# Kernel optimization log

Measured on AMD Instinct MI355X. Metric: run time of the kernel, lower is better.

The kernel has to match this reference:

```python
import jax, jax.numpy as jnp
import numpy as np

NBINS = 256
STRENGTH = 100.0  # __init__ strength kwarg


def _hist_channel(x):
    # x: [N] flattened masked channel -> 256-bin histogram over [min,max]
    lo = jnp.min(x)
    hi = jnp.max(x)
    scale = (NBINS - 1) / jnp.maximum(hi - lo, 1e-12)
    bins = jnp.clip(jnp.floor((x - lo) * scale + 0.5).astype(jnp.int32), 0, NBINS - 1)
    return jnp.zeros((NBINS,), dtype=x.dtype).at[bins].add(1.0)


def _match_channel(x, t_hist):
    # CDF-based histogram matching (cpp.matchHistogram): remap sorted values of x
    # to bin centers of the target histogram; output normalized to [0,1].
    N = x.shape[0]
    idx = jnp.argsort(x)
    t = t_hist * (N / jnp.maximum(jnp.sum(t_hist), 1e-12))
    cdf = jnp.cumsum(t)  # [NBINS]
    ranks = jnp.arange(N, dtype=cdf.dtype) + 0.5
    bins = jnp.clip(jnp.searchsorted(cdf, ranks), 0, NBINS - 1)
    vals = bins.astype(x.dtype) / (NBINS - 1)
    return jnp.zeros_like(x).at[idx].set(vals)


def reference(input, masks, target_hists, target_mins, target_maxs):
    # input: [1,C,H,W]; masks: [S,H,W]; target_hists: [S,C,256]; mins/maxs: [S,C]
    C = input.shape[1]
    x = input[0]  # [C,H,W]

    def per_style(mask, t_hist, t_min, t_max):
        mf = (x * mask[None]).reshape(C, -1)  # masked feature, [C,N]
        hist = jax.vmap(_hist_channel)(mf)    # computed every call (as in source)
        matched = jax.vmap(_match_channel)(mf, t_hist)  # [C,N] in [0,1]
        target = matched * (t_max - t_min)[:, None] + t_min[:, None]
        target = jax.lax.stop_gradient(target)  # torch uses .data (detached)
        loss = 0.01 * STRENGTH * jnp.mean((mf - target) ** 2)  # nn.MSELoss
        return loss, hist

    losses, hists = jax.vmap(per_style)(masks, target_hists, target_mins, target_maxs)
    return jnp.sum(losses), hists


def setup_inputs() -> dict:
    key = jax.random.key(0)
    k1, k2, k3, k4 = jax.random.split(key, 4)
    S, C, H, W = 2, 256, 256, 256
    input = jax.random.normal(k1, (1, C, H, W), dtype=jnp.float32)
    masks = (jax.random.uniform(k2, (S, H, W)) > 0.5).astype(jnp.float32)
    target_hists = jax.random.uniform(k3, (S, C, NBINS), dtype=jnp.float32) * 100.0
    base = jax.random.normal(k4, (S, C), dtype=jnp.float32)
    target_mins = base - 1.0
    target_maxs = base + 1.0
    return {"input": input, "masks": masks, "target_hists": target_hists,
            "target_mins": target_mins, "target_maxs": target_maxs}
```

## Files before the change

kernel.cpp:

```cpp
#include <hip/hip_runtime.h>
#include <math.h>

#define NBINS 256
#define NB    4096
#define NCOPY 4
#define BLKT  1024

__global__ void mask_bits_kernel(const float* __restrict__ masks,
                                 unsigned* __restrict__ bits, int total)
{
    const int idx = blockIdx.x * blockDim.x + threadIdx.x;
    bool m = false;
    if (idx < total) m = (masks[idx] != 0.0f);
    const unsigned long long b = __ballot(m);
    const int lane = threadIdx.x & 63;
    if (idx < total) {
        if (lane == 0)       bits[idx >> 5] = (unsigned)b;
        else if (lane == 32) bits[idx >> 5] = (unsigned)(b >> 32);
    }
}

__global__ __launch_bounds__(BLKT, 8) void fused_kernel(
    const float* __restrict__ x, const unsigned* __restrict__ bits,
    const float* __restrict__ thist, const float* __restrict__ tmins,
    const float* __restrict__ tmaxs,
    float* __restrict__ out, float* __restrict__ lossws, int C, int N)
{
    const int nwg = gridDim.x;
    const int orig = blockIdx.x;
    int newid = orig;
    if ((nwg & 7) == 0) newid = (orig & 7) * (nwg >> 3) + (orig >> 3);
    const int c = newid >> 1;
    const int g = newid & 1;

    const float* __restrict__ xc = x + (size_t)c * N;
    const unsigned* __restrict__ wb = bits + (size_t)g * (N >> 5);
    const int tid = threadIdx.x, lane = tid & 63, wid = tid >> 6;

    __shared__ unsigned cntS[NCOPY][NB + 1];
    __shared__ float Sarr[NBINS];
    __shared__ int   Karr[NBINS];
    __shared__ float thsum[4];
    __shared__ unsigned ctot[16];
    __shared__ float wtot[16];
    __shared__ float lsum[4];
    __shared__ float statsS[3];
    __shared__ float wr[3][16];

    const int step16 = BLKT * 16;
    const int Nmain  = (N / step16) * step16;

    float mn = 3.4e38f, mx = -3.4e38f, sq = 0.f;
    for (int i = tid * 16; i < Nmain; i += step16) {
        const float4 a0 = *reinterpret_cast<const float4*>(xc + i);
        const float4 a1 = *reinterpret_cast<const float4*>(xc + i + 4);
        const float4 a2 = *reinterpret_cast<const float4*>(xc + i + 8);
        const float4 a3 = *reinterpret_cast<const float4*>(xc + i + 12);
        const unsigned w = wb[i >> 5] >> (i & 31);
        const float e[16] = { a0.x, a0.y, a0.z, a0.w, a1.x, a1.y, a1.z, a1.w,
                              a2.x, a2.y, a2.z, a2.w, a3.x, a3.y, a3.z, a3.w };
        #pragma unroll
        for (int j = 0; j < 16; ++j) {
            const float v = ((w >> j) & 1u) ? e[j] : 0.0f;
            mn = fminf(mn, v); mx = fmaxf(mx, v); sq += v * v;
        }
    }
    for (int i = Nmain + tid * 4; i < N; i += BLKT * 4) {
        const float4 xv = *reinterpret_cast<const float4*>(xc + i);
        const unsigned w = wb[i >> 5] >> (i & 31);
        const float e[4] = { xv.x, xv.y, xv.z, xv.w };
        #pragma unroll
        for (int j = 0; j < 4; ++j) {
            const float v = ((w >> j) & 1u) ? e[j] : 0.0f;
            mn = fminf(mn, v); mx = fmaxf(mx, v); sq += v * v;
        }
    }
    #pragma unroll
    for (int off = 32; off > 0; off >>= 1) {
        mn = fminf(mn, __shfl_xor(mn, off));
        mx = fmaxf(mx, __shfl_xor(mx, off));
        sq += __shfl_xor(sq, off);
    }
    if (lane == 0) { wr[0][wid] = mn; wr[1][wid] = mx; wr[2][wid] = sq; }

    float th = 0.f, thscan = 0.f;
    if (tid < NBINS) {
        th = thist[(size_t)(g * C + c) * NBINS + tid];
        thscan = th;
        #pragma unroll
        for (int off = 1; off < 64; off <<= 1) {
            const float t = __shfl_up(thscan, off);
            if (lane >= off) thscan += t;
        }
        if (lane == 63) thsum[wid] = thscan;
    }
    {
        unsigned* cf = &cntS[0][0];
        for (int k = tid; k < NCOPY * (NB + 1); k += BLKT) cf[k] = 0u;
    }
    __syncthreads();

    if (tid == 0) {
        float a = wr[0][0], b = wr[1][0], s = wr[2][0];
        for (int k = 1; k < 16; ++k) {
            a = fminf(a, wr[0][k]); b = fmaxf(b, wr[1][k]); s += wr[2][k];
        }
        statsS[0] = a; statsS[1] = b; statsS[2] = s;
    }
    __syncthreads();

    const float lo   = statsS[0];
    const float rng  = fmaxf(statsS[1] - lo, 1e-12f);
    const float sc16 = 4080.0f / rng;
    const float u    = rng / 4080.0f;

    if (tid < NBINS) {
        float cross = 0.f, tsum = 0.f;
        #pragma unroll
        for (int w2 = 0; w2 < 4; ++w2) { if (w2 < wid) cross += thsum[w2]; tsum += thsum[w2]; }
        const float scale = (float)N / fmaxf(tsum, 1e-12f);
        const float cdfv = (thscan + cross) * scale;
        int K = (int)floorf(cdfv - 0.5f) + 1;
        K = min(N, max(0, K));
        if (tid == NBINS - 1) K = N;
        Karr[tid] = K;
    }

    unsigned* __restrict__ cm = cntS[wid >> 2];
    for (int i = tid * 16; i < Nmain; i += step16) {
        const float4 a0 = *reinterpret_cast<const float4*>(xc + i);
        const float4 a1 = *reinterpret_cast<const float4*>(xc + i + 4);
        const float4 a2 = *reinterpret_cast<const float4*>(xc + i + 8);
        const float4 a3 = *reinterpret_cast<const float4*>(xc + i + 12);
        const unsigned w = wb[i >> 5] >> (i & 31);
        const float e[16] = { a0.x, a0.y, a0.z, a0.w, a1.x, a1.y, a1.z, a1.w,
                              a2.x, a2.y, a2.z, a2.w, a3.x, a3.y, a3.z, a3.w };
        #pragma unroll
        for (int j = 0; j < 16; ++j) {
            if ((w >> j) & 1u) {
                const int jb = min(NB - 1, max(0, (int)floorf((e[j] - lo) * sc16 + 8.0f)));
                atomicAdd(&cm[jb], 1u);
            }
        }
    }
    for (int i = Nmain + tid * 4; i < N; i += BLKT * 4) {
        const float4 xv = *reinterpret_cast<const float4*>(xc + i);
        const unsigned w = wb[i >> 5] >> (i & 31);
        const float e[4] = { xv.x, xv.y, xv.z, xv.w };
        #pragma unroll
        for (int j = 0; j < 4; ++j) {
            if ((w >> j) & 1u) {
                const int jb = min(NB - 1, max(0, (int)floorf((e[j] - lo) * sc16 + 8.0f)));
                atomicAdd(&cm[jb], 1u);
            }
        }
    }
    __syncthreads();

    const int b4 = tid * 4;
    unsigned c_[4]; float w_[4];
    unsigned csum = 0u; float wsum = 0.f;
    #pragma unroll
    for (int q2 = 0; q2 < 4; ++q2) {
        unsigned cc = cntS[0][b4 + q2];
        #pragma unroll
        for (int cp2 = 1; cp2 < NCOPY; ++cp2) cc += cntS[cp2][b4 + q2];
        c_[q2] = cc;
        w_[q2] = (float)cc * ((float)(b4 + q2) - 7.5f);
        csum += cc; wsum += w_[q2];
    }
    unsigned cin = csum; float win = wsum;
    #pragma unroll
    for (int off = 1; off < 64; off <<= 1) {
        const unsigned cu = __shfl_up(cin, off);
        const float    wu = __shfl_up(win, off);
        if (lane >= off) { cin += cu; win += wu; }
    }
    if (lane == 63) { ctot[wid] = cin; wtot[wid] = win; }
    __syncthreads();
    unsigned cofs = 0u; float wofs = 0.f;
    #pragma unroll
    for (int w2 = 0; w2 < 16; ++w2)
        if (w2 < wid) { cofs += ctot[w2]; wofs += wtot[w2]; }
    unsigned cex = cofs + (cin - csum);
    float    wex = wofs + (win - wsum);
    {
        unsigned* __restrict__ cp = cntS[0];
        float*    __restrict__ WF = (float*)cntS[1];
        #pragma unroll
        for (int q2 = 0; q2 < 4; ++q2) {
            cp[b4 + q2] = cex; WF[b4 + q2] = wex;
            cex += c_[q2]; wex += w_[q2];
        }
        if (tid == BLKT - 1) { cp[NB] = cex; WF[NB] = wex; }
    }
    __syncthreads();

    if (tid < NBINS) {
        const float schist = 255.0f / rng;
        unsigned* __restrict__ cp = cntS[0];
        float*    __restrict__ WF = (float*)cntS[1];
        const unsigned n0 = (unsigned)N - cp[NB];
        const int ib0 = min(NBINS - 1, max(0, (int)floorf((0.0f - lo) * schist + 0.5f)));
        const int b0  = min(NB - 1,    max(0, (int)floorf((0.0f - lo) * sc16 + 8.0f)));

        unsigned h = cp[16 * tid + 16] - cp[16 * tid];
        if (tid == ib0) h += n0;
        out[1 + (size_t)(g * C + c) * NBINS + tid] = (float)h;

        const unsigned Z0 = cp[b0];
        const unsigned k = (unsigned)Karr[tid];
        float Sv;
        if (tid == NBINS - 1) {
            Sv = lo * (float)cp[NB] + u * WF[NB];
        } else if (k <= Z0) {
            int jlo = 0, jhi = b0;
            while (jlo < jhi) { const int mid = (jlo + jhi + 1) >> 1;
                if (cp[mid] <= k) jlo = mid; else jhi = mid - 1; }
            const unsigned d = k - cp[jlo];
            Sv = lo * (float)k + u * (WF[jlo] + (float)d * ((float)jlo - 7.5f));
        } else if (k <= Z0 + n0) {
            Sv = lo * (float)Z0 + u * WF[b0];
        } else {
            const unsigned k2 = k - n0;
            int jlo = b0, jhi = NB;
            while (jlo < jhi) { const int mid = (jlo + jhi + 1) >> 1;
                if (cp[mid] <= k2) jlo = mid; else jhi = mid - 1; }
            const unsigned d = k2 - cp[jlo];
            Sv = lo * (float)k2 + u * (WF[jlo] + (float)d * ((float)jlo - 7.5f));
        }
        Sarr[tid] = Sv;
    }
    __syncthreads();

    float term = 0.f;
    if (tid < NBINS) {
        const float tmn = tmins[g * C + c], tmx = tmaxs[g * C + c];
        const float Tb = ((float)tid / 255.0f) * (tmx - tmn) + tmn;
        const float Sb = Sarr[tid];
        const float Sp = (tid == 0) ? 0.f : Sarr[tid - 1];
        const int   Kb = Karr[tid];
        const int   Kp = (tid == 0) ? 0 : Karr[tid - 1];
        term = -2.0f * Tb * (Sb - Sp) + Tb * Tb * (float)(Kb - Kp);
    }
    #pragma unroll
    for (int off = 32; off > 0; off >>= 1) term += __shfl_xor(term, off);
    if (lane == 0 && wid < 4) lsum[wid] = term;
    __syncthreads();
    if (tid == 0) {
        const float t = (lsum[0] + lsum[1]) + (lsum[2] + lsum[3]);
        lossws[g * C + c] = (statsS[2] + t) / ((float)C * (float)N);
    }
}

__global__ void reduce_loss_kernel(const float* __restrict__ lossws,
                                   float* __restrict__ out, int n)
{
    __shared__ float sh[256];
    const int tid = threadIdx.x;
    float v = 0.f;
    for (int i = tid; i < n; i += 256) v += lossws[i];
    sh[tid] = v;
    __syncthreads();
    for (int st = 128; st > 0; st >>= 1) {
        if (tid < st) sh[tid] += sh[tid + st];
        __syncthreads();
    }
    if (tid == 0) out[0] = sh[0];
}

extern "C" void kernel_launch(void* const* d_in, const int* in_sizes, int n_in,
                              void* d_out, int out_size, void* d_ws, size_t ws_size,
                              hipStream_t stream)
{
    const float* x     = (const float*)d_in[0];
    const float* masks = (const float*)d_in[1];
    const float* thist = (const float*)d_in[2];
    const float* tmins = (const float*)d_in[3];
    const float* tmaxs = (const float*)d_in[4];
    float* out = (float*)d_out;

    const int SC = in_sizes[3];
    const long long ratio = (long long)in_sizes[0] / (long long)in_sizes[1];
    const long long csq   = (long long)SC * ratio;
    const int C = (int)(sqrt((double)csq) + 0.5);
    const int S = SC / C;
    const int N = in_sizes[1] / S;
    const int total = in_sizes[1];

    float* lossws = (float*)d_ws;
    const size_t off1 = ((size_t)SC * 4 + 255) & ~(size_t)255;
    unsigned* bits = (unsigned*)((char*)d_ws + off1);

    mask_bits_kernel<<<(total + 1023) / 1024, 1024, 0, stream>>>(masks, bits, total);
    fused_kernel<<<S * C, BLKT, 0, stream>>>(x, bits, thist, tmins, tmaxs,
                                             out, lossws, C, N);
    reduce_loss_kernel<<<1, 256, 0, stream>>>(lossws, out, SC);
}
```

Baseline: 40.70 us.

## Halve block size, software-prefetch streaming loops, and drop bin clamping

Each workgroup drops from 1024 to 512 threads with two histogram copies instead of four, and the prefix-scan stage now has each thread handle 8 bins. Both streaming passes over the channel now load the next 16-element chunk into registers before processing the current one, so global loads overlap with the reductions and atomics. The bin index now uses an fmaf without floor or clamping, which removes a few ALU ops per element but assumes values always fall inside the valid range. Fewer threads per block lowers per-block parallelism in exchange for more occupancy and less shared-memory contention across blocks, and the extra prefetch registers add register pressure.

```diff
diff --git a/kernel.cpp b/kernel.cpp
--- a/kernel.cpp
+++ b/kernel.cpp
@@ -3,8 +3,9 @@
 
 #define NBINS 256
 #define NB    4096
-#define NCOPY 4
-#define BLKT  1024
+#define NCOPY 2
+#define BLKT  512
+#define NWAVE (BLKT / 64)
 
 __global__ void mask_bits_kernel(const float* __restrict__ masks,
                                  unsigned* __restrict__ bits, int total)
@@ -41,28 +42,45 @@
     __shared__ float Sarr[NBINS];
     __shared__ int   Karr[NBINS];
     __shared__ float thsum[4];
-    __shared__ unsigned ctot[16];
-    __shared__ float wtot[16];
+    __shared__ unsigned ctot[NWAVE];
+    __shared__ float wtot[NWAVE];
     __shared__ float lsum[4];
     __shared__ float statsS[3];
-    __shared__ float wr[3][16];
+    __shared__ float wr[3][NWAVE];
 
     const int step16 = BLKT * 16;
     const int Nmain  = (N / step16) * step16;
+    const int niter  = Nmain / step16;
 
     float mn = 3.4e38f, mx = -3.4e38f, sq = 0.f;
-    for (int i = tid * 16; i < Nmain; i += step16) {
-        const float4 a0 = *reinterpret_cast<const float4*>(xc + i);
-        const float4 a1 = *reinterpret_cast<const float4*>(xc + i + 4);
-        const float4 a2 = *reinterpret_cast<const float4*>(xc + i + 8);
-        const float4 a3 = *reinterpret_cast<const float4*>(xc + i + 12);
-        const unsigned w = wb[i >> 5] >> (i & 31);
-        const float e[16] = { a0.x, a0.y, a0.z, a0.w, a1.x, a1.y, a1.z, a1.w,
-                              a2.x, a2.y, a2.z, a2.w, a3.x, a3.y, a3.z, a3.w };
-        #pragma unroll
-        for (int j = 0; j < 16; ++j) {
-            const float v = ((w >> j) & 1u) ? e[j] : 0.0f;
-            mn = fminf(mn, v); mx = fmaxf(mx, v); sq += v * v;
+    {
+        int i = tid * 16;
+        float4 a0, a1, a2, a3; unsigned w = 0;
+        if (niter > 0) {
+            a0 = *reinterpret_cast<const float4*>(xc + i);
+            a1 = *reinterpret_cast<const float4*>(xc + i + 4);
+            a2 = *reinterpret_cast<const float4*>(xc + i + 8);
+            a3 = *reinterpret_cast<const float4*>(xc + i + 12);
+            w  = wb[i >> 5] >> (i & 31);
+        }
+        for (int it = 0; it < niter; ++it) {
+            float4 b0, b1, b2, b3; unsigned wn = 0;
+            const int inext = i + step16;
+            if (it + 1 < niter) {
+                b0 = *reinterpret_cast<const float4*>(xc + inext);
+                b1 = *reinterpret_cast<const float4*>(xc + inext + 4);
+                b2 = *reinterpret_cast<const float4*>(xc + inext + 8);
+                b3 = *reinterpret_cast<const float4*>(xc + inext + 12);
+                wn = wb[inext >> 5] >> (inext & 31);
+            }
+            const float e[16] = { a0.x, a0.y, a0.z, a0.w, a1.x, a1.y, a1.z, a1.w,
+                                  a2.x, a2.y, a2.z, a2.w, a3.x, a3.y, a3.z, a3.w };
+            #pragma unroll
+            for (int j = 0; j < 16; ++j) {
+                const float v = ((w >> j) & 1u) ? e[j] : 0.0f;
+                mn = fminf(mn, v); mx = fmaxf(mx, v); sq = fmaf(v, v, sq);
+            }
+            a0 = b0; a1 = b1; a2 = b2; a3 = b3; w = wn; i = inext;
         }
     }
     for (int i = Nmain + tid * 4; i < N; i += BLKT * 4) {
@@ -72,7 +90,7 @@
         #pragma unroll
         for (int j = 0; j < 4; ++j) {
             const float v = ((w >> j) & 1u) ? e[j] : 0.0f;
-            mn = fminf(mn, v); mx = fmaxf(mx, v); sq += v * v;
+            mn = fminf(mn, v); mx = fmaxf(mx, v); sq = fmaf(v, v, sq);
         }
     }
     #pragma unroll
@@ -102,7 +120,7 @@
 
     if (tid == 0) {
         float a = wr[0][0], b = wr[1][0], s = wr[2][0];
-        for (int k = 1; k < 16; ++k) {
+        for (int k = 1; k < NWAVE; ++k) {
             a = fminf(a, wr[0][k]); b = fmaxf(b, wr[1][k]); s += wr[2][k];
         }
         statsS[0] = a; statsS[1] = b; statsS[2] = s;
@@ -127,20 +145,36 @@
     }
 
     unsigned* __restrict__ cm = cntS[wid >> 2];
-    for (int i = tid * 16; i < Nmain; i += step16) {
-        const float4 a0 = *reinterpret_cast<const float4*>(xc + i);
-        const float4 a1 = *reinterpret_cast<const float4*>(xc + i + 4);
-        const float4 a2 = *reinterpret_cast<const float4*>(xc + i + 8);
-        const float4 a3 = *reinterpret_cast<const float4*>(xc + i + 12);
-        const unsigned w = wb[i >> 5] >> (i & 31);
-        const float e[16] = { a0.x, a0.y, a0.z, a0.w, a1.x, a1.y, a1.z, a1.w,
-                              a2.x, a2.y, a2.z, a2.w, a3.x, a3.y, a3.z, a3.w };
-        #pragma unroll
-        for (int j = 0; j < 16; ++j) {
-            if ((w >> j) & 1u) {
-                const int jb = min(NB - 1, max(0, (int)floorf((e[j] - lo) * sc16 + 8.0f)));
-                atomicAdd(&cm[jb], 1u);
-            }
+    {
+        int i = tid * 16;
+        float4 a0, a1, a2, a3; unsigned w = 0;
+        if (niter > 0) {
+            a0 = *reinterpret_cast<const float4*>(xc + i);
+            a1 = *reinterpret_cast<const float4*>(xc + i + 4);
+            a2 = *reinterpret_cast<const float4*>(xc + i + 8);
+            a3 = *reinterpret_cast<const float4*>(xc + i + 12);
+            w  = wb[i >> 5] >> (i & 31);
+        }
+        for (int it = 0; it < niter; ++it) {
+            float4 b0, b1, b2, b3; unsigned wn = 0;
+            const int inext = i + step16;
+            if (it + 1 < niter) {
+                b0 = *reinterpret_cast<const float4*>(xc + inext);
+                b1 = *reinterpret_cast<const float4*>(xc + inext + 4);
+                b2 = *reinterpret_cast<const float4*>(xc + inext + 8);
+                b3 = *reinterpret_cast<const float4*>(xc + inext + 12);
+                wn = wb[inext >> 5] >> (inext & 31);
+            }
+            const float e[16] = { a0.x, a0.y, a0.z, a0.w, a1.x, a1.y, a1.z, a1.w,
+                                  a2.x, a2.y, a2.z, a2.w, a3.x, a3.y, a3.z, a3.w };
+            #pragma unroll
+            for (int j = 0; j < 16; ++j) {
+                if ((w >> j) & 1u) {
+                    const int jb = (int)fmaf(e[j] - lo, sc16, 8.0f);
+                    atomicAdd(&cm[jb], 1u);
+                }
+            }
+            a0 = b0; a1 = b1; a2 = b2; a3 = b3; w = wn; i = inext;
         }
     }
     for (int i = Nmain + tid * 4; i < N; i += BLKT * 4) {
@@ -150,23 +184,23 @@
         #pragma unroll
         for (int j = 0; j < 4; ++j) {
             if ((w >> j) & 1u) {
-                const int jb = min(NB - 1, max(0, (int)floorf((e[j] - lo) * sc16 + 8.0f)));
+                const int jb = (int)fmaf(e[j] - lo, sc16, 8.0f);
                 atomicAdd(&cm[jb], 1u);
             }
         }
     }
     __syncthreads();
 
-    const int b4 = tid * 4;
-    unsigned c_[4]; float w_[4];
+    const int b8 = tid * 8;
+    unsigned c_[8]; float w_[8];
     unsigned csum = 0u; float wsum = 0.f;
     #pragma unroll
-    for (int q2 = 0; q2 < 4; ++q2) {
-        unsigned cc = cntS[0][b4 + q2];
-        #pragma unroll
-        for (int cp2 = 1; cp2 < NCOPY; ++cp2) cc += cntS[cp2][b4 + q2];
+    for (int q2 = 0; q2 < 8; ++q2) {
+        unsigned cc = cntS[0][b8 + q2];
+        #pragma unroll
+        for (int cp2 = 1; cp2 < NCOPY; ++cp2) cc += cntS[cp2][b8 + q2];
         c_[q2] = cc;
-        w_[q2] = (float)cc * ((float)(b4 + q2) - 7.5f);
+        w_[q2] = (float)cc * ((float)(b8 + q2) - 7.5f);
         csum += cc; wsum += w_[q2];
     }
     unsigned cin = csum; float win = wsum;
@@ -180,7 +214,7 @@
     __syncthreads();
     unsigned cofs = 0u; float wofs = 0.f;
     #pragma unroll
-    for (int w2 = 0; w2 < 16; ++w2)
+    for (int w2 = 0; w2 < NWAVE; ++w2)
         if (w2 < wid) { cofs += ctot[w2]; wofs += wtot[w2]; }
     unsigned cex = cofs + (cin - csum);
     float    wex = wofs + (win - wsum);
@@ -188,8 +222,8 @@
         unsigned* __restrict__ cp = cntS[0];
         float*    __restrict__ WF = (float*)cntS[1];
         #pragma unroll
-        for (int q2 = 0; q2 < 4; ++q2) {
-            cp[b4 + q2] = cex; WF[b4 + q2] = wex;
+        for (int q2 = 0; q2 < 8; ++q2) {
+            cp[b8 + q2] = cex; WF[b8 + q2] = wex;
             cex += c_[q2]; wex += w_[q2];
         }
         if (tid == BLKT - 1) { cp[NB] = cex; WF[NB] = wex; }
```

Measured after the change: 43.12 us. 5.9% more time.

## Split min/max/sumsq pass into a separate multi-block stats kernel shared across styles

Applied to the files above, without the earlier changes.

Moves the per-channel masked min/max/sum-of-squares pass out of the fused kernel into a stats kernel. That kernel splits each channel across 8 blocks and computes both styles' masks from a single read of x. The match kernel then combines the partial stats and runs only the histogram and matching pass, so one block-wide barrier and one of the two full reads of x per block go away. It also drops the clamp on the bin index and uses an fma, relying on the computed min/max to keep indices in range. The cost is an extra kernel launch and a global round-trip for the partial stats. The stats loop also has no tail handling when a segment is not a multiple of 4096 elements.

```diff
diff --git a/kernel.cpp b/kernel.cpp
--- a/kernel.cpp
+++ b/kernel.cpp
@@ -5,6 +5,7 @@
 #define NB    4096
 #define NCOPY 4
 #define BLKT  1024
+#define PSPL  8
 
 __global__ void mask_bits_kernel(const float* __restrict__ masks,
                                  unsigned* __restrict__ bits, int total)
@@ -20,8 +21,68 @@
     }
 }
 
-__global__ __launch_bounds__(BLKT, 8) void fused_kernel(
+__global__ __launch_bounds__(256, 8) void stats_kernel(
     const float* __restrict__ x, const unsigned* __restrict__ bits,
+    float4* __restrict__ pstats, int C, int N)
+{
+    const int blk = blockIdx.x;
+    const int c = blk / PSPL, p = blk - c * PSPL;
+    const float* __restrict__ xc = x + (size_t)c * N;
+    const unsigned* __restrict__ wb0 = bits;
+    const unsigned* __restrict__ wb1 = bits + (N >> 5);
+    const int tid = threadIdx.x, lane = tid & 63, wid = tid >> 6;
+    const int seg = N / PSPL;
+    const int base = p * seg, end = base + seg;
+    __shared__ float wr[6][4];
+
+    float mn0 = 3.4e38f, mx0 = -3.4e38f, sq0 = 0.f;
+    float mn1 = 3.4e38f, mx1 = -3.4e38f, sq1 = 0.f;
+    const int step16 = 256 * 16;
+    for (int i = base + tid * 16; i + 15 < end; i += step16) {
+        const float4 a0 = *reinterpret_cast<const float4*>(xc + i);
+        const float4 a1 = *reinterpret_cast<const float4*>(xc + i + 4);
+        const float4 a2 = *reinterpret_cast<const float4*>(xc + i + 8);
+        const float4 a3 = *reinterpret_cast<const float4*>(xc + i + 12);
+        const unsigned w0 = wb0[i >> 5] >> (i & 31);
+        const unsigned w1 = wb1[i >> 5] >> (i & 31);
+        const float e[16] = { a0.x, a0.y, a0.z, a0.w, a1.x, a1.y, a1.z, a1.w,
+                              a2.x, a2.y, a2.z, a2.w, a3.x, a3.y, a3.z, a3.w };
+        #pragma unroll
+        for (int j = 0; j < 16; ++j) {
+            const float v0 = ((w0 >> j) & 1u) ? e[j] : 0.0f;
+            const float v1 = ((w1 >> j) & 1u) ? e[j] : 0.0f;
+            mn0 = fminf(mn0, v0); mx0 = fmaxf(mx0, v0); sq0 = fmaf(v0, v0, sq0);
+            mn1 = fminf(mn1, v1); mx1 = fmaxf(mx1, v1); sq1 = fmaf(v1, v1, sq1);
+        }
+    }
+    #pragma unroll
+    for (int off = 32; off > 0; off >>= 1) {
+        mn0 = fminf(mn0, __shfl_xor(mn0, off));
+        mx0 = fmaxf(mx0, __shfl_xor(mx0, off));
+        sq0 += __shfl_xor(sq0, off);
+        mn1 = fminf(mn1, __shfl_xor(mn1, off));
+        mx1 = fmaxf(mx1, __shfl_xor(mx1, off));
+        sq1 += __shfl_xor(sq1, off);
+    }
+    if (lane == 0) {
+        wr[0][wid] = mn0; wr[1][wid] = mx0; wr[2][wid] = sq0;
+        wr[3][wid] = mn1; wr[4][wid] = mx1; wr[5][wid] = sq1;
+    }
+    __syncthreads();
+    if (tid < 2) {
+        const int b6 = tid * 3;
+        float mn = wr[b6 + 0][0], mx = wr[b6 + 1][0], sq = wr[b6 + 2][0];
+        for (int k = 1; k < 4; ++k) {
+            mn = fminf(mn, wr[b6 + 0][k]); mx = fmaxf(mx, wr[b6 + 1][k]);
+            sq += wr[b6 + 2][k];
+        }
+        pstats[tid * (C * PSPL) + blk] = make_float4(mn, mx, sq, 0.f);
+    }
+}
+
+__global__ __launch_bounds__(BLKT, 8) void match_kernel(
+    const float* __restrict__ x, const unsigned* __restrict__ bits,
+    const float4* __restrict__ pstats,
     const float* __restrict__ thist, const float* __restrict__ tmins,
     const float* __restrict__ tmaxs,
     float* __restrict__ out, float* __restrict__ lossws, int C, int N)
@@ -45,12 +106,55 @@
     __shared__ float wtot[16];
     __shared__ float lsum[4];
     __shared__ float statsS[3];
-    __shared__ float wr[3][16];
-
+
+    if (tid == 0) {
+        const float4* pp = pstats + (size_t)g * (C * PSPL) + (size_t)c * PSPL;
+        float4 p0 = pp[0];
+        float mn = p0.x, mx = p0.y, sq = p0.z;
+        #pragma unroll
+        for (int k = 1; k < PSPL; ++k) {
+            const float4 pk = pp[k];
+            mn = fminf(mn, pk.x); mx = fmaxf(mx, pk.y); sq += pk.z;
+        }
+        statsS[0] = mn; statsS[1] = mx; statsS[2] = sq;
+    }
+    float th = 0.f, thscan = 0.f;
+    if (tid < NBINS) {
+        th = thist[(size_t)(g * C + c) * NBINS + tid];
+        thscan = th;
+        #pragma unroll
+        for (int off = 1; off < 64; off <<= 1) {
+            const float t = __shfl_up(thscan, off);
+            if (lane >= off) thscan += t;
+        }
+        if (lane == 63) thsum[wid] = thscan;
+    }
+    {
+        unsigned* cf = &cntS[0][0];
+        for (int k = tid; k < NCOPY * (NB + 1); k += BLKT) cf[k] = 0u;
+    }
+    __syncthreads();
+
+    const float lo   = statsS[0];
+    const float rng  = fmaxf(statsS[1] - lo, 1e-12f);
+    const float sc16 = 4080.0f / rng;
+    const float u    = rng / 4080.0f;
+
+    if (tid < NBINS) {
+        float cross = 0.f, tsum = 0.f;
+        #pragma unroll
+        for (int w2 = 0; w2 < 4; ++w2) { if (w2 < wid) cross += thsum[w2]; tsum += thsum[w2]; }
+        const float scale = (float)N / fmaxf(tsum, 1e-12f);
+        const float cdfv = (thscan + cross) * scale;
+        int K = (int)floorf(cdfv - 0.5f) + 1;
+        K = min(N, max(0, K));
+        if (tid == NBINS - 1) K = N;
+        Karr[tid] = K;
+    }
+
+    unsigned* __restrict__ cm = cntS[wid >> 2];
     const int step16 = BLKT * 16;
     const int Nmain  = (N / step16) * step16;
-
-    float mn = 3.4e38f, mx = -3.4e38f, sq = 0.f;
     for (int i = tid * 16; i < Nmain; i += step16) {
         const float4 a0 = *reinterpret_cast<const float4*>(xc + i);
         const float4 a1 = *reinterpret_cast<const float4*>(xc + i + 4);
@@ -61,8 +165,10 @@
                               a2.x, a2.y, a2.z, a2.w, a3.x, a3.y, a3.z, a3.w };
         #pragma unroll
         for (int j = 0; j < 16; ++j) {
-            const float v = ((w >> j) & 1u) ? e[j] : 0.0f;
-            mn = fminf(mn, v); mx = fmaxf(mx, v); sq += v * v;
+            if ((w >> j) & 1u) {
+                const int jb = (int)fmaf(e[j] - lo, sc16, 8.0f);
+                atomicAdd(&cm[jb], 1u);
+            }
         }
     }
     for (int i = Nmain + tid * 4; i < N; i += BLKT * 4) {
@@ -71,86 +177,8 @@
         const float e[4] = { xv.x, xv.y, xv.z, xv.w };
         #pragma unroll
         for (int j = 0; j < 4; ++j) {
-            const float v = ((w >> j) & 1u) ? e[j] : 0.0f;
-            mn = fminf(mn, v); mx = fmaxf(mx, v); sq += v * v;
-        }
-    }
-    #pragma unroll
-    for (int off = 32; off > 0; off >>= 1) {
-        mn = fminf(mn, __shfl_xor(mn, off));
-        mx = fmaxf(mx, __shfl_xor(mx, off));
-        sq += __shfl_xor(sq, off);
-    }
-    if (lane == 0) { wr[0][wid] = mn; wr[1][wid] = mx; wr[2][wid] = sq; }
-
-    float th = 0.f, thscan = 0.f;
-    if (tid < NBINS) {
-        th = thist[(size_t)(g * C + c) * NBINS + tid];
-        thscan = th;
-        #pragma unroll
-        for (int off = 1; off < 64; off <<= 1) {
-            const float t = __shfl_up(thscan, off);
-            if (lane >= off) thscan += t;
-        }
-        if (lane == 63) thsum[wid] = thscan;
-    }
-    {
-        unsigned* cf = &cntS[0][0];
-        for (int k = tid; k < NCOPY * (NB + 1); k += BLKT) cf[k] = 0u;
-    }
-    __syncthreads();
-
-    if (tid == 0) {
-        float a = wr[0][0], b = wr[1][0], s = wr[2][0];
-        for (int k = 1; k < 16; ++k) {
-            a = fminf(a, wr[0][k]); b = fmaxf(b, wr[1][k]); s += wr[2][k];
-        }
-        statsS[0] = a; statsS[1] = b; statsS[2] = s;
-    }
-    __syncthreads();
-
-    const float lo   = statsS[0];
-    const float rng  = fmaxf(statsS[1] - lo, 1e-12f);
-    const float sc16 = 4080.0f / rng;
-    const float u    = rng / 4080.0f;
-
-    if (tid < NBINS) {
-        float cross = 0.f, tsum = 0.f;
-        #pragma unroll
-        for (int w2 = 0; w2 < 4; ++w2) { if (w2 < wid) cross += thsum[w2]; tsum += thsum[w2]; }
-        const float scale = (float)N / fmaxf(tsum, 1e-12f);
-        const float cdfv = (thscan + cross) * scale;
-        int K = (int)floorf(cdfv - 0.5f) + 1;
-        K = min(N, max(0, K));
-        if (tid == NBINS - 1) K = N;
-        Karr[tid] = K;
-    }
-
-    unsigned* __restrict__ cm = cntS[wid >> 2];
-    for (int i = tid * 16; i < Nmain; i += step16) {
-        const float4 a0 = *reinterpret_cast<const float4*>(xc + i);
-        const float4 a1 = *reinterpret_cast<const float4*>(xc + i + 4);
-        const float4 a2 = *reinterpret_cast<const float4*>(xc + i + 8);
-        const float4 a3 = *reinterpret_cast<const float4*>(xc + i + 12);
-        const unsigned w = wb[i >> 5] >> (i & 31);
-        const float e[16] = { a0.x, a0.y, a0.z, a0.w, a1.x, a1.y, a1.z, a1.w,
-                              a2.x, a2.y, a2.z, a2.w, a3.x, a3.y, a3.z, a3.w };
-        #pragma unroll
-        for (int j = 0; j < 16; ++j) {
             if ((w >> j) & 1u) {
-                const int jb = min(NB - 1, max(0, (int)floorf((e[j] - lo) * sc16 + 8.0f)));
-                atomicAdd(&cm[jb], 1u);
-            }
-        }
-    }
-    for (int i = Nmain + tid * 4; i < N; i += BLKT * 4) {
-        const float4 xv = *reinterpret_cast<const float4*>(xc + i);
-        const unsigned w = wb[i >> 5] >> (i & 31);
-        const float e[4] = { xv.x, xv.y, xv.z, xv.w };
-        #pragma unroll
-        for (int j = 0; j < 4; ++j) {
-            if ((w >> j) & 1u) {
-                const int jb = min(NB - 1, max(0, (int)floorf((e[j] - lo) * sc16 + 8.0f)));
+                const int jb = (int)fmaf(e[j] - lo, sc16, 8.0f);
                 atomicAdd(&cm[jb], 1u);
             }
         }
@@ -290,10 +318,13 @@
 
     float* lossws = (float*)d_ws;
     const size_t off1 = ((size_t)SC * 4 + 255) & ~(size_t)255;
-    unsigned* bits = (unsigned*)((char*)d_ws + off1);
+    float4* pstats = (float4*)((char*)d_ws + off1);
+    const size_t off2 = (off1 + (size_t)S * C * PSPL * 16 + 255) & ~(size_t)255;
+    unsigned* bits = (unsigned*)((char*)d_ws + off2);
 
     mask_bits_kernel<<<(total + 1023) / 1024, 1024, 0, stream>>>(masks, bits, total);
-    fused_kernel<<<S * C, BLKT, 0, stream>>>(x, bits, thist, tmins, tmaxs,
+    stats_kernel<<<C * PSPL, 256, 0, stream>>>(x, bits, pstats, C, N);
+    match_kernel<<<S * C, BLKT, 0, stream>>>(x, bits, pstats, thist, tmins, tmaxs,
                                              out, lossws, C, N);
     reduce_loss_kernel<<<1, 256, 0, stream>>>(lossws, out, SC);
 }
```

New measurement: 45.84 us. 1.13x slower.

## Fuse final loss reduction via last-block counter and trim stats pass arithmetic

Applied to the files above, without the earlier changes.

Removes the separate reduce kernel: each block writes its per-channel loss, bumps a global counter reset in the mask kernel, and the last block to finish sums all losses. The sum of squares moves from the min/max pass into the histogram pass, and the min/max pass uses a tree reduction instead of a serial chain. The bin-index clamp and floor are dropped in favour of an fma plus truncation, which relies on the index always staying in range. This saves one kernel launch and some ALU work per element, at the cost of atomics, threadfences and a tail reduction done by one block.

```diff
diff --git a/kernel.cpp b/kernel.cpp
--- a/kernel.cpp
+++ b/kernel.cpp
@@ -7,8 +7,10 @@
 #define BLKT  1024
 
 __global__ void mask_bits_kernel(const float* __restrict__ masks,
-                                 unsigned* __restrict__ bits, int total)
+                                 unsigned* __restrict__ bits,
+                                 unsigned* __restrict__ ctr, int total)
 {
+    if (blockIdx.x == 0 && threadIdx.x == 0) *ctr = 0u;
     const int idx = blockIdx.x * blockDim.x + threadIdx.x;
     bool m = false;
     if (idx < total) m = (masks[idx] != 0.0f);
@@ -24,7 +26,8 @@
     const float* __restrict__ x, const unsigned* __restrict__ bits,
     const float* __restrict__ thist, const float* __restrict__ tmins,
     const float* __restrict__ tmaxs,
-    float* __restrict__ out, float* __restrict__ lossws, int C, int N)
+    float* __restrict__ out, float* __restrict__ lossws,
+    unsigned* __restrict__ ctr, int C, int N)
 {
     const int nwg = gridDim.x;
     const int orig = blockIdx.x;
@@ -46,11 +49,12 @@
     __shared__ float lsum[4];
     __shared__ float statsS[3];
     __shared__ float wr[3][16];
+    __shared__ unsigned lastFlag;
 
     const int step16 = BLKT * 16;
     const int Nmain  = (N / step16) * step16;
 
-    float mn = 3.4e38f, mx = -3.4e38f, sq = 0.f;
+    float mn = 3.4e38f, mx = -3.4e38f;
     for (int i = tid * 16; i < Nmain; i += step16) {
         const float4 a0 = *reinterpret_cast<const float4*>(xc + i);
         const float4 a1 = *reinterpret_cast<const float4*>(xc + i + 4);
@@ -59,11 +63,21 @@
         const unsigned w = wb[i >> 5] >> (i & 31);
         const float e[16] = { a0.x, a0.y, a0.z, a0.w, a1.x, a1.y, a1.z, a1.w,
                               a2.x, a2.y, a2.z, a2.w, a3.x, a3.y, a3.z, a3.w };
-        #pragma unroll
-        for (int j = 0; j < 16; ++j) {
-            const float v = ((w >> j) & 1u) ? e[j] : 0.0f;
-            mn = fminf(mn, v); mx = fmaxf(mx, v); sq += v * v;
-        }
+        float s[16];
+        #pragma unroll
+        for (int j = 0; j < 16; ++j) s[j] = ((w >> j) & 1u) ? e[j] : 0.0f;
+        const float nA = fminf(fminf(s[0], s[1]), s[2]);
+        const float nB = fminf(fminf(s[3], s[4]), s[5]);
+        const float nC = fminf(fminf(s[6], s[7]), s[8]);
+        const float nD = fminf(fminf(s[9], s[10]), s[11]);
+        const float nE = fminf(fminf(s[12], s[13]), s[14]);
+        mn = fminf(mn, fminf(fminf(fminf(nA, nB), nC), fminf(fminf(nD, nE), s[15])));
+        const float xA = fmaxf(fmaxf(s[0], s[1]), s[2]);
+        const float xB = fmaxf(fmaxf(s[3], s[4]), s[5]);
+        const float xC = fmaxf(fmaxf(s[6], s[7]), s[8]);
+        const float xD = fmaxf(fmaxf(s[9], s[10]), s[11]);
+        const float xE = fmaxf(fmaxf(s[12], s[13]), s[14]);
+        mx = fmaxf(mx, fmaxf(fmaxf(fmaxf(xA, xB), xC), fmaxf(fmaxf(xD, xE), s[15])));
     }
     for (int i = Nmain + tid * 4; i < N; i += BLKT * 4) {
         const float4 xv = *reinterpret_cast<const float4*>(xc + i);
@@ -72,16 +86,15 @@
         #pragma unroll
         for (int j = 0; j < 4; ++j) {
             const float v = ((w >> j) & 1u) ? e[j] : 0.0f;
-            mn = fminf(mn, v); mx = fmaxf(mx, v); sq += v * v;
+            mn = fminf(mn, v); mx = fmaxf(mx, v);
         }
     }
     #pragma unroll
     for (int off = 32; off > 0; off >>= 1) {
         mn = fminf(mn, __shfl_xor(mn, off));
         mx = fmaxf(mx, __shfl_xor(mx, off));
-        sq += __shfl_xor(sq, off);
-    }
-    if (lane == 0) { wr[0][wid] = mn; wr[1][wid] = mx; wr[2][wid] = sq; }
+    }
+    if (lane == 0) { wr[0][wid] = mn; wr[1][wid] = mx; }
 
     float th = 0.f, thscan = 0.f;
     if (tid < NBINS) {
@@ -101,11 +114,9 @@
     __syncthreads();
 
     if (tid == 0) {
-        float a = wr[0][0], b = wr[1][0], s = wr[2][0];
-        for (int k = 1; k < 16; ++k) {
-            a = fminf(a, wr[0][k]); b = fmaxf(b, wr[1][k]); s += wr[2][k];
-        }
-        statsS[0] = a; statsS[1] = b; statsS[2] = s;
+        float a = wr[0][0], b = wr[1][0];
+        for (int k = 1; k < 16; ++k) { a = fminf(a, wr[0][k]); b = fmaxf(b, wr[1][k]); }
+        statsS[0] = a; statsS[1] = b;
     }
     __syncthreads();
 
@@ -127,6 +138,7 @@
     }
 
     unsigned* __restrict__ cm = cntS[wid >> 2];
+    float sq = 0.f;
     for (int i = tid * 16; i < Nmain; i += step16) {
         const float4 a0 = *reinterpret_cast<const float4*>(xc + i);
         const float4 a1 = *reinterpret_cast<const float4*>(xc + i + 4);
@@ -138,8 +150,9 @@
         #pragma unroll
         for (int j = 0; j < 16; ++j) {
             if ((w >> j) & 1u) {
-                const int jb = min(NB - 1, max(0, (int)floorf((e[j] - lo) * sc16 + 8.0f)));
+                const int jb = (int)fmaf(e[j] - lo, sc16, 8.0f);
                 atomicAdd(&cm[jb], 1u);
+                sq = fmaf(e[j], e[j], sq);
             }
         }
     }
@@ -150,12 +163,21 @@
         #pragma unroll
         for (int j = 0; j < 4; ++j) {
             if ((w >> j) & 1u) {
-                const int jb = min(NB - 1, max(0, (int)floorf((e[j] - lo) * sc16 + 8.0f)));
+                const int jb = (int)fmaf(e[j] - lo, sc16, 8.0f);
                 atomicAdd(&cm[jb], 1u);
+                sq = fmaf(e[j], e[j], sq);
             }
         }
     }
-    __syncthreads();
+    #pragma unroll
+    for (int off = 32; off > 0; off >>= 1) sq += __shfl_xor(sq, off);
+    if (lane == 0) wr[2][wid] = sq;
+    __syncthreads();
+    if (tid == 0) {
+        float s = wr[2][0];
+        for (int k = 1; k < 16; ++k) s += wr[2][k];
+        statsS[2] = s;
+    }
 
     const int b4 = tid * 4;
     unsigned c_[4]; float w_[4];
@@ -247,26 +269,30 @@
     for (int off = 32; off > 0; off >>= 1) term += __shfl_xor(term, off);
     if (lane == 0 && wid < 4) lsum[wid] = term;
     __syncthreads();
+
     if (tid == 0) {
         const float t = (lsum[0] + lsum[1]) + (lsum[2] + lsum[3]);
-        lossws[g * C + c] = (statsS[2] + t) / ((float)C * (float)N);
-    }
-}
-
-__global__ void reduce_loss_kernel(const float* __restrict__ lossws,
-                                   float* __restrict__ out, int n)
-{
-    __shared__ float sh[256];
-    const int tid = threadIdx.x;
-    float v = 0.f;
-    for (int i = tid; i < n; i += 256) v += lossws[i];
-    sh[tid] = v;
-    __syncthreads();
-    for (int st = 128; st > 0; st >>= 1) {
-        if (tid < st) sh[tid] += sh[tid + st];
+        const float lossv = (statsS[2] + t) / ((float)C * (float)N);
+        atomicExch(&lossws[g * C + c], lossv);
+        __threadfence();
+        const unsigned prev = atomicAdd(ctr, 1u);
+        lastFlag = (prev == (unsigned)(nwg - 1)) ? 1u : 0u;
+    }
+    __syncthreads();
+    if (lastFlag) {
+        __threadfence();
+        float v = 0.f;
+        for (int i = tid; i < nwg; i += BLKT) v += lossws[i];
+        #pragma unroll
+        for (int off = 32; off > 0; off >>= 1) v += __shfl_xor(v, off);
+        if (lane == 0) wtot[wid] = v;
         __syncthreads();
-    }
-    if (tid == 0) out[0] = sh[0];
+        if (tid == 0) {
+            float tt = 0.f;
+            for (int k = 0; k < 16; ++k) tt += wtot[k];
+            out[0] = tt;
+        }
+    }
 }
 
 extern "C" void kernel_launch(void* const* d_in, const int* in_sizes, int n_in,
@@ -290,10 +316,11 @@
 
     float* lossws = (float*)d_ws;
     const size_t off1 = ((size_t)SC * 4 + 255) & ~(size_t)255;
-    unsigned* bits = (unsigned*)((char*)d_ws + off1);
-
-    mask_bits_kernel<<<(total + 1023) / 1024, 1024, 0, stream>>>(masks, bits, total);
+    unsigned* ctr = (unsigned*)((char*)d_ws + off1);
+    const size_t off2 = (off1 + 256 + 255) & ~(size_t)255;
+    unsigned* bits = (unsigned*)((char*)d_ws + off2);
+
+    mask_bits_kernel<<<(total + 1023) / 1024, 1024, 0, stream>>>(masks, bits, ctr, total);
     fused_kernel<<<S * C, BLKT, 0, stream>>>(x, bits, thist, tmins, tmaxs,
-                                             out, lossws, C, N);
-    reduce_loss_kernel<<<1, 256, 0, stream>>>(lossws, out, SC);
+                                             out, lossws, ctr, C, N);
 }
```

Result: slower. 56.24 us (+38.2%).
